# Kernel tuning notes

Measured on AMD Instinct MI355X. Metric: run time of the kernel, lower is better.

The kernel has to match this reference:

```python
import jax, jax.numpy as jnp
import numpy as np
import math

N_HEADS = 16
D_KV = 64
D_MODEL = 1024
NUM_BUCKETS = 32
MAX_DISTANCE = 128


def _relative_position_bucket(rel_pos):
    # encoder (is_decoder=False): bidirectional buckets
    num_buckets = NUM_BUCKETS // 2  # 16
    rel_buckets = (rel_pos > 0).astype(jnp.int32) * num_buckets
    rel_pos = jnp.abs(rel_pos)
    max_exact = num_buckets // 2  # 8
    is_small = rel_pos < max_exact
    rel_pos_large = max_exact + (
        jnp.log(rel_pos.astype(jnp.float32) / max_exact)
        / math.log(MAX_DISTANCE / max_exact)
        * (num_buckets - max_exact)
    ).astype(jnp.int32)
    rel_pos_large = jnp.minimum(rel_pos_large, num_buckets - 1)
    return rel_buckets + jnp.where(is_small, rel_pos, rel_pos_large)


def setup_inputs() -> dict:
    key = jax.random.key(0)
    ks = jax.random.split(key, 6)
    s = 1.0 / math.sqrt(D_MODEL)
    return {
        "hidden_states": jax.random.normal(ks[0], (2, 2048, D_MODEL), jnp.float32),
        "Wq": jax.random.normal(ks[1], (D_MODEL, N_HEADS * D_KV), jnp.float32) * s,
        "Wk": jax.random.normal(ks[2], (D_MODEL, N_HEADS * D_KV), jnp.float32) * s,
        "Wv": jax.random.normal(ks[3], (D_MODEL, N_HEADS * D_KV), jnp.float32) * s,
        "Wo": jax.random.normal(ks[4], (N_HEADS * D_KV, D_MODEL), jnp.float32) * s,
        "rel_bias": jax.random.normal(ks[5], (NUM_BUCKETS, N_HEADS), jnp.float32),
    }


def reference(hidden_states, Wq, Wk, Wv, Wo, rel_bias):
    b, seq, _ = hidden_states.shape
    q = (hidden_states @ Wq).reshape(b, seq, N_HEADS, D_KV)
    k = (hidden_states @ Wk).reshape(b, seq, N_HEADS, D_KV)
    v = (hidden_states @ Wv).reshape(b, seq, N_HEADS, D_KV)

    # relative position bias: [1, n_heads, q_len, k_len]
    ctx = jnp.arange(seq, dtype=jnp.int32)[:, None]
    mem = jnp.arange(seq, dtype=jnp.int32)[None, :]
    buckets = _relative_position_bucket(mem - ctx)  # [q, k]
    pos_bias = rel_bias[buckets]                    # [q, k, h]
    pos_bias = jnp.transpose(pos_bias, (2, 0, 1))[None]  # [1, h, q, k]

    # NOTE: T5-style attention has no 1/sqrt(d) scaling
    attn = jnp.einsum('binc,bjnc->bnij', q, k) + pos_bias
    attn = jax.nn.softmax(attn.astype(jnp.float32), axis=-1).astype(attn.dtype)
    o = jnp.einsum('bnij,bjnc->binc', attn, v).reshape(b, seq, N_HEADS * D_KV)
    return o @ Wo
```

## Files before the change

kernel.cpp:

```cpp
#include <hip/hip_runtime.h>
#include <hip/hip_bf16.h>
#include <math.h>

#define DM   1024
#define HD   1024
#define NH   16
#define DK   64
#define SEQ  2048
#define BATCH 2

typedef __attribute__((ext_vector_type(8))) short bf16x8;
typedef __attribute__((ext_vector_type(4))) float f32x4;

static __device__ __forceinline__ short f2b(float f) {
  union { float f; unsigned u; } v; v.f = f;
  unsigned r = (v.u + 0x7fffu + ((v.u >> 16) & 1u)) >> 16;
  return (short)r;
}

static __device__ __forceinline__ void gload_lds16(const void* g, void* l) {
  __builtin_amdgcn_global_load_lds(
      (const __attribute__((address_space(1))) void*)g,
      (__attribute__((address_space(3))) void*)l, 16, 0, 0);
}


__global__ __launch_bounds__(256) void k_cvt_h(const float* __restrict__ in,
                                               short* __restrict__ out) {
  int i = (blockIdx.x * 256 + threadIdx.x) * 8;
  float4 a = *reinterpret_cast<const float4*>(in + i);
  float4 b = *reinterpret_cast<const float4*>(in + i + 4);
  bf16x8 o;
  o[0] = f2b(a.x); o[1] = f2b(a.y); o[2] = f2b(a.z); o[3] = f2b(a.w);
  o[4] = f2b(b.x); o[5] = f2b(b.y); o[6] = f2b(b.z); o[7] = f2b(b.w);
  *reinterpret_cast<bf16x8*>(out + i) = o;
}

__global__ __launch_bounds__(256) void k_wtrans(const float* __restrict__ Wq,
                                                const float* __restrict__ Wk,
                                                const float* __restrict__ Wv,
                                                const float* __restrict__ Wo,
                                                short* __restrict__ Wts) {
  const float* src = (blockIdx.z == 0) ? Wq : (blockIdx.z == 1) ? Wk
                   : (blockIdx.z == 2) ? Wv : Wo;
  short* dst = Wts + (size_t)blockIdx.z * DM * HD;
  __shared__ float t[32][33];
  int tx = threadIdx.x & 31, ty = threadIdx.x >> 5;
  int k0 = blockIdx.y * 32, n0 = blockIdx.x * 32;
#pragma unroll
  for (int i = 0; i < 4; ++i)
    t[ty + i * 8][tx] = src[(size_t)(k0 + ty + i * 8) * 1024 + n0 + tx];
  __syncthreads();
#pragma unroll
  for (int i = 0; i < 4; ++i)
    dst[(size_t)(n0 + ty + i * 8) * 1024 + k0 + tx] = f2b(t[tx][ty + i * 8]);
}

__global__ __launch_bounds__(256) void k_bias(const float* __restrict__ rel_bias,
                                              float* __restrict__ btab) {
  int idx = blockIdx.x * 256 + threadIdx.x;
  int h = idx >> 12, pos = idx & 4095;
  int delta = pos - 2047;
  int rb = (delta > 0) ? 16 : 0;
  int ar = (delta < 0) ? -delta : delta;
  int bb;
  if (ar < 8) bb = ar;
  else {
    bb = 8 + (int)(logf((float)ar * 0.125f) * (8.0f / 2.7725887222397811f));
    if (bb > 15) bb = 15;
  }
  btab[idx] = rel_bias[(rb + bb) * NH + h];
}

__global__ __launch_bounds__(256) void k_vtrans(const short* __restrict__ Vb,
                                                short* __restrict__ Vt) {
  int bh = blockIdx.y, b = bh >> 4, h = bh & 15;
  int st = blockIdx.x * 64;
  __shared__ short t[64][72];
  int tx = threadIdx.x & 15, ty = threadIdx.x >> 4;
#pragma unroll
  for (int i = 0; i < 4; ++i) {
    int row = ty + i * 16;
    *reinterpret_cast<short4*>(&t[row][tx * 4]) =
        *reinterpret_cast<const short4*>(
            &Vb[(size_t)(b * SEQ + st + row) * HD + h * 64 + tx * 4]);
  }
  __syncthreads();
#pragma unroll
  for (int i = 0; i < 4; ++i) {
    int dk = ty + i * 16;
    short4 v = make_short4(t[tx * 4 + 0][dk], t[tx * 4 + 1][dk],
                           t[tx * 4 + 2][dk], t[tx * 4 + 3][dk]);
    *reinterpret_cast<short4*>(
        &Vt[(size_t)bh * DK * SEQ + (size_t)dk * SEQ + st + tx * 4]) = v;
  }
}

template <int OUTF32>
__global__ __launch_bounds__(256) void k_gemm_bt(const short* __restrict__ A,
                                                 const short* __restrict__ Bt,
                                                 void* __restrict__ Cv,
                                                 size_t btz, size_t cz) {
  __shared__ __align__(16) short As[128 * 32];
  __shared__ __align__(16) short Bs[128 * 32];
  const int tid = threadIdx.x, w = tid >> 6, lane = tid & 63;
  const int wr = w >> 1, wc = w & 1, lg = lane >> 4, l15 = lane & 15;
  const int rowBase = blockIdx.y * 128, colBase = blockIdx.x * 128;
  const short* B = Bt + (size_t)blockIdx.z * btz;

  f32x4 acc[4][4];
#pragma unroll
  for (int m = 0; m < 4; ++m)
#pragma unroll
    for (int n = 0; n < 4; ++n) acc[m][n] = (f32x4){0.f, 0.f, 0.f, 0.f};

  const int c1 = w * 64 + lane, c2 = c1 + 256;
  const short* Ap1 = A + (size_t)(rowBase + (c1 >> 2)) * 1024 + (c1 & 3) * 8;
  const short* Ap2 = A + (size_t)(rowBase + (c2 >> 2)) * 1024 + (c2 & 3) * 8;
  const short* Bp1 = B + (size_t)(colBase + (c1 >> 2)) * 1024 + (c1 & 3) * 8;
  const short* Bp2 = B + (size_t)(colBase + (c2 >> 2)) * 1024 + (c2 & 3) * 8;
  char* AsB = (char*)As;
  char* BsB = (char*)Bs;

  for (int k0 = 0; k0 < 1024; k0 += 32) {
    __syncthreads();
    gload_lds16(Ap1 + k0, AsB + w * 1024);
    gload_lds16(Ap2 + k0, AsB + 4096 + w * 1024);
    gload_lds16(Bp1 + k0, BsB + w * 1024);
    gload_lds16(Bp2 + k0, BsB + 4096 + w * 1024);
    asm volatile("s_waitcnt vmcnt(0)" ::: "memory");
    __syncthreads();
    bf16x8 af[4], bfr[4];
#pragma unroll
    for (int m = 0; m < 4; ++m)
      af[m] = *reinterpret_cast<const bf16x8*>(
          &As[(wr * 64 + m * 16 + l15) * 32 + lg * 8]);
#pragma unroll
    for (int n = 0; n < 4; ++n)
      bfr[n] = *reinterpret_cast<const bf16x8*>(
          &Bs[(wc * 64 + n * 16 + l15) * 32 + lg * 8]);
#pragma unroll
    for (int m = 0; m < 4; ++m)
#pragma unroll
      for (int n = 0; n < 4; ++n)
        acc[m][n] =
            __builtin_amdgcn_mfma_f32_16x16x32_bf16(af[m], bfr[n], acc[m][n], 0, 0, 0);
  }

#pragma unroll
  for (int m = 0; m < 4; ++m)
#pragma unroll
    for (int n = 0; n < 4; ++n) {
      int col = colBase + wc * 64 + n * 16 + l15;
#pragma unroll
      for (int r = 0; r < 4; ++r) {
        int row = rowBase + wr * 64 + m * 16 + lg * 4 + r;
        if (OUTF32)
          ((float*)Cv)[(size_t)row * 1024 + col] = acc[m][n][r];
        else
          ((short*)Cv + (size_t)blockIdx.z * cz)[(size_t)row * 1024 + col] =
              f2b(acc[m][n][r]);
      }
    }
}

static __device__ __forceinline__ void stage_tile(const char* gbase, size_t grs,
                                                  char* lbase, int w, int lane) {
  const int r0 = w * 16 + (lane >> 3);
  const int cb = (lane & 7) * 16;
  const int sw = (r0 & 7) << 4;
  gload_lds16(gbase + (size_t)r0 * grs + (cb ^ sw), lbase + w * 2048);
  gload_lds16(gbase + (size_t)(r0 + 8) * grs + (cb ^ sw), lbase + w * 2048 + 1024);
}

__global__ __launch_bounds__(256, 4) void k_attn(const short* __restrict__ Qb,
                                                 const short* __restrict__ Kb,
                                                 const short* __restrict__ Vt,
                                                 const float* __restrict__ biasTab,
                                                 short* __restrict__ Ob) {
  const int j = blockIdx.x;
  const int orig = (j & 7) * 128 + (j >> 3);
  const int qt = orig & 31, bh = orig >> 5;
  const int b = bh >> 4, h = bh & 15;
  const int w = threadIdx.x >> 6, lane = threadIdx.x & 63;
  const int lg = lane >> 4, l15 = lane & 15;
  const int qbase = qt * 64 + w * 16;

  __shared__ __align__(16) char Ks[2][8192];
  __shared__ __align__(16) char Vs[2][8192];
  __shared__ __align__(16) short Plds[4][1024];
  char* PwB = (char*)(&Plds[w][0]);
  const int swz = (l15 & 7) << 4;

  const short* Qrow = Qb + (size_t)(b * SEQ + qbase + l15) * HD + h * 64 + lg * 8;
  bf16x8 q0 = *reinterpret_cast<const bf16x8*>(Qrow);
  bf16x8 q1 = *reinterpret_cast<const bf16x8*>(Qrow + 32);

  const char* Kg = (const char*)(Kb + (size_t)(b * SEQ) * HD + h * 64);
  const char* Vg = (const char*)(Vt + (size_t)bh * DK * SEQ);
  const float* btab = biasTab + h * 4096 + 2047;
  const float bias_hi = btab[1024];
  const float bias_lo = btab[-1024];

  f32x4 o[4];
#pragma unroll
  for (int c = 0; c < 4; ++c) o[c] = (f32x4){0.f, 0.f, 0.f, 0.f};
  float m_r = -INFINITY, l_r = 0.f;

  const f32x4 z4 = (f32x4){0.f, 0.f, 0.f, 0.f};
  const int rb0 = (l15 * 128 + lg * 16) ^ swz;
  const int rb1 = (l15 * 128 + 64 + lg * 16) ^ swz;

  stage_tile(Kg, 2048, Ks[0], w, lane);
  stage_tile(Vg, 4096, Vs[0], w, lane);
  asm volatile("s_waitcnt vmcnt(0)" ::: "memory");
  __syncthreads();
  int cur = 0;

  for (int kt = 0; kt < 32; ++kt) {
    const int kvb = kt * 64;
    const int dkv = kvb - qbase;
    if (kt < 31) {
      stage_tile(Kg + (size_t)(kvb + 64) * 2048, 2048, Ks[cur ^ 1], w, lane);
      stage_tile(Vg + (size_t)(kvb + 64) * 2, 4096, Vs[cur ^ 1], w, lane);
    }
    const char* KsC = Ks[cur];
    f32x4 s[4];
#pragma unroll
    for (int c = 0; c < 4; ++c) {
      const int krow = c * 16 + l15;
      const int ksw = (krow & 7) << 4;
      const char* kr = KsC + krow * 128;
      bf16x8 kf0 = *reinterpret_cast<const bf16x8*>(kr + ((lg * 16) ^ ksw));
      bf16x8 kf1 = *reinterpret_cast<const bf16x8*>(kr + ((64 + lg * 16) ^ ksw));
      s[c] = __builtin_amdgcn_mfma_f32_16x16x32_bf16(kf0, q0, z4, 0, 0, 0);
      s[c] = __builtin_amdgcn_mfma_f32_16x16x32_bf16(kf1, q1, s[c], 0, 0, 0);
    }
    if (dkv >= 112) {
#pragma unroll
      for (int c = 0; c < 4; ++c)
#pragma unroll
        for (int r = 0; r < 4; ++r) s[c][r] += bias_hi;
    } else if (dkv <= -160) {
#pragma unroll
      for (int c = 0; c < 4; ++c)
#pragma unroll
        for (int r = 0; r < 4; ++r) s[c][r] += bias_lo;
    } else {
#pragma unroll
      for (int c = 0; c < 4; ++c)
#pragma unroll
        for (int r = 0; r < 4; ++r)
          s[c][r] += btab[dkv + c * 16 + lg * 4 + r - l15];
    }
    float mx = s[0][0];
#pragma unroll
    for (int c = 0; c < 4; ++c)
#pragma unroll
      for (int r = 0; r < 4; ++r) mx = fmaxf(mx, s[c][r]);
    mx = fmaxf(mx, __shfl_xor(mx, 16, 64));
    mx = fmaxf(mx, __shfl_xor(mx, 32, 64));
    float mn = fmaxf(m_r, mx);
    float sc = __expf(m_r - mn);
    m_r = mn;
    float rs = 0.f;
#pragma unroll
    for (int c = 0; c < 4; ++c)
#pragma unroll
      for (int r = 0; r < 4; ++r) {
        float p = __expf(s[c][r] - m_r);
        s[c][r] = p;
        rs += p;
      }
    rs += __shfl_xor(rs, 16, 64);
    rs += __shfl_xor(rs, 32, 64);
    l_r = l_r * sc + rs;
#pragma unroll
    for (int c = 0; c < 4; ++c)
#pragma unroll
      for (int r = 0; r < 4; ++r) o[c][r] *= sc;
#pragma unroll
    for (int c = 0; c < 4; ++c) {
      short4 pk;
      pk.x = f2b(s[c][0]); pk.y = f2b(s[c][1]);
      pk.z = f2b(s[c][2]); pk.w = f2b(s[c][3]);
      int byte = (l15 * 128 + c * 32 + lg * 8) ^ swz;
      *reinterpret_cast<short4*>(PwB + byte) = pk;
    }
    const char* VsC = Vs[cur];
    bf16x8 vf0[4], vf1[4];
#pragma unroll
    for (int c = 0; c < 4; ++c) {
      const int vrow = c * 16 + l15;
      const int vsw = (vrow & 7) << 4;
      const char* vr = VsC + vrow * 128;
      vf0[c] = *reinterpret_cast<const bf16x8*>(vr + ((lg * 16) ^ vsw));
      vf1[c] = *reinterpret_cast<const bf16x8*>(vr + ((64 + lg * 16) ^ vsw));
    }
    asm volatile("s_waitcnt lgkmcnt(0)" ::: "memory");
    bf16x8 pb0 = *reinterpret_cast<const bf16x8*>(PwB + rb0);
    bf16x8 pb1 = *reinterpret_cast<const bf16x8*>(PwB + rb1);
#pragma unroll
    for (int c = 0; c < 4; ++c) {
      o[c] = __builtin_amdgcn_mfma_f32_16x16x32_bf16(vf0[c], pb0, o[c], 0, 0, 0);
      o[c] = __builtin_amdgcn_mfma_f32_16x16x32_bf16(vf1[c], pb1, o[c], 0, 0, 0);
    }
    asm volatile("s_waitcnt vmcnt(0)" ::: "memory");
    __syncthreads();
    cur ^= 1;
  }
  float inv = 1.0f / l_r;
  const size_t orow = (size_t)(b * SEQ + qbase + l15) * HD + h * 64;
#pragma unroll
  for (int c = 0; c < 4; ++c) {
    short4 pk;
    pk.x = f2b(o[c][0] * inv); pk.y = f2b(o[c][1] * inv);
    pk.z = f2b(o[c][2] * inv); pk.w = f2b(o[c][3] * inv);
    *reinterpret_cast<short4*>(&Ob[orow + c * 16 + lg * 4]) = pk;
  }
}

extern "C" void kernel_launch(void* const* d_in, const int* in_sizes, int n_in,
                              void* d_out, int out_size, void* d_ws, size_t ws_size,
                              hipStream_t stream) {
  const float* H    = (const float*)d_in[0];
  const float* Wq   = (const float*)d_in[1];
  const float* Wk   = (const float*)d_in[2];
  const float* Wv   = (const float*)d_in[3];
  const float* Wo   = (const float*)d_in[4];
  const float* relb = (const float*)d_in[5];

  char* ws = (char*)d_ws;
  short* Hb   = (short*)(ws);
  short* Wts  = (short*)(ws + ((size_t)8 << 20));
  short* Qb   = (short*)(ws + ((size_t)16 << 20));
  short* Kb   = (short*)(ws + ((size_t)24 << 20));
  short* Vb   = (short*)(ws + ((size_t)32 << 20));
  short* Vt   = (short*)(ws + ((size_t)40 << 20));
  short* Ob   = (short*)(ws + ((size_t)48 << 20));
  float* btab = (float*)(ws + ((size_t)56 << 20));

  k_cvt_h<<<2048, 256, 0, stream>>>(H, Hb);
  k_wtrans<<<dim3(32, 32, 4), 256, 0, stream>>>(Wq, Wk, Wv, Wo, Wts);
  k_bias<<<256, 256, 0, stream>>>(relb, btab);

  k_gemm_bt<0><<<dim3(8, 32, 3), 256, 0, stream>>>(
      Hb, Wts, Qb, (size_t)1024 * 1024, (size_t)4096 * 1024);

  k_vtrans<<<dim3(32, 32), 256, 0, stream>>>(Vb, Vt);
  k_attn<<<1024, 256, 0, stream>>>(Qb, Kb, Vt, btab, Ob);

  k_gemm_bt<1><<<dim3(8, 32, 1), 256, 0, stream>>>(
      Ob, Wts + (size_t)3 * 1024 * 1024, d_out, 0, 0);
}
```

Before: 223.6 us.

## Keep softmax probabilities in registers and use exp2 with lazy rescaling in attention

Folds log2(e) into the Q weight and the bias table so the attention kernel can use exp2 directly. It removes the per-wave LDS round trip for the P matrix by packing probabilities straight into MFMA operands and reading V with a matching permuted layout. It also skips the running-max rescale of the output accumulators unless the new max exceeds the old one by more than a threshold. The LDS footprint and waits shrink, at the cost of more LDS read instructions (short4 loads) for V and a relaxed-max softmax that trusts the threshold to avoid overflow.

```diff
diff --git a/kernel.cpp b/kernel.cpp
--- a/kernel.cpp
+++ b/kernel.cpp
@@ -8,6 +8,8 @@
 #define DK   64
 #define SEQ  2048
 #define BATCH 2
+
+#define LOG2E 1.4426950408889634f
 
 typedef __attribute__((ext_vector_type(8))) short bf16x8;
 typedef __attribute__((ext_vector_type(4))) float f32x4;
@@ -43,6 +45,7 @@
                                                 short* __restrict__ Wts) {
   const float* src = (blockIdx.z == 0) ? Wq : (blockIdx.z == 1) ? Wk
                    : (blockIdx.z == 2) ? Wv : Wo;
+  const float scl = (blockIdx.z == 0) ? LOG2E : 1.0f;
   short* dst = Wts + (size_t)blockIdx.z * DM * HD;
   __shared__ float t[32][33];
   int tx = threadIdx.x & 31, ty = threadIdx.x >> 5;
@@ -53,7 +56,7 @@
   __syncthreads();
 #pragma unroll
   for (int i = 0; i < 4; ++i)
-    dst[(size_t)(n0 + ty + i * 8) * 1024 + k0 + tx] = f2b(t[tx][ty + i * 8]);
+    dst[(size_t)(n0 + ty + i * 8) * 1024 + k0 + tx] = f2b(t[tx][ty + i * 8] * scl);
 }
 
 __global__ __launch_bounds__(256) void k_bias(const float* __restrict__ rel_bias,
@@ -69,7 +72,7 @@
     bb = 8 + (int)(logf((float)ar * 0.125f) * (8.0f / 2.7725887222397811f));
     if (bb > 15) bb = 15;
   }
-  btab[idx] = rel_bias[(rb + bb) * NH + h];
+  btab[idx] = rel_bias[(rb + bb) * NH + h] * LOG2E;
 }
 
 __global__ __launch_bounds__(256) void k_vtrans(const short* __restrict__ Vb,
@@ -188,8 +191,6 @@
 
   __shared__ __align__(16) char Ks[2][8192];
   __shared__ __align__(16) char Vs[2][8192];
-  __shared__ __align__(16) short Plds[4][1024];
-  char* PwB = (char*)(&Plds[w][0]);
   const int swz = (l15 & 7) << 4;
 
   const short* Qrow = Qb + (size_t)(b * SEQ + qbase + l15) * HD + h * 64 + lg * 8;
@@ -208,8 +209,6 @@
   float m_r = -INFINITY, l_r = 0.f;
 
   const f32x4 z4 = (f32x4){0.f, 0.f, 0.f, 0.f};
-  const int rb0 = (l15 * 128 + lg * 16) ^ swz;
-  const int rb1 = (l15 * 128 + 64 + lg * 16) ^ swz;
 
   stage_tile(Kg, 2048, Ks[0], w, lane);
   stage_tile(Vg, 4096, Vs[0], w, lane);
@@ -228,11 +227,9 @@
     f32x4 s[4];
 #pragma unroll
     for (int c = 0; c < 4; ++c) {
-      const int krow = c * 16 + l15;
-      const int ksw = (krow & 7) << 4;
-      const char* kr = KsC + krow * 128;
-      bf16x8 kf0 = *reinterpret_cast<const bf16x8*>(kr + ((lg * 16) ^ ksw));
-      bf16x8 kf1 = *reinterpret_cast<const bf16x8*>(kr + ((64 + lg * 16) ^ ksw));
+      const char* kr = KsC + (c * 16 + l15) * 128;
+      bf16x8 kf0 = *reinterpret_cast<const bf16x8*>(kr + ((lg * 16) ^ swz));
+      bf16x8 kf1 = *reinterpret_cast<const bf16x8*>(kr + ((64 + lg * 16) ^ swz));
       s[c] = __builtin_amdgcn_mfma_f32_16x16x32_bf16(kf0, q0, z4, 0, 0, 0);
       s[c] = __builtin_amdgcn_mfma_f32_16x16x32_bf16(kf1, q1, s[c], 0, 0, 0);
     }
@@ -253,57 +250,58 @@
         for (int r = 0; r < 4; ++r)
           s[c][r] += btab[dkv + c * 16 + lg * 4 + r - l15];
     }
-    float mx = s[0][0];
-#pragma unroll
-    for (int c = 0; c < 4; ++c)
-#pragma unroll
-      for (int r = 0; r < 4; ++r) mx = fmaxf(mx, s[c][r]);
+    float t0 = fmaxf(fmaxf(s[0][0], s[0][1]), fmaxf(s[0][2], s[0][3]));
+    float t1 = fmaxf(fmaxf(s[1][0], s[1][1]), fmaxf(s[1][2], s[1][3]));
+    float t2 = fmaxf(fmaxf(s[2][0], s[2][1]), fmaxf(s[2][2], s[2][3]));
+    float t3 = fmaxf(fmaxf(s[3][0], s[3][1]), fmaxf(s[3][2], s[3][3]));
+    float mx = fmaxf(fmaxf(t0, t1), fmaxf(t2, t3));
     mx = fmaxf(mx, __shfl_xor(mx, 16, 64));
     mx = fmaxf(mx, __shfl_xor(mx, 32, 64));
-    float mn = fmaxf(m_r, mx);
-    float sc = __expf(m_r - mn);
-    m_r = mn;
-    float rs = 0.f;
+    if (!__all(mx <= m_r + 8.0f)) {
+      float mn = fmaxf(m_r, mx);
+      float sc = __builtin_exp2f(m_r - mn);
+      m_r = mn;
+      l_r *= sc;
+#pragma unroll
+      for (int c = 0; c < 4; ++c)
+#pragma unroll
+        for (int r = 0; r < 4; ++r) o[c][r] *= sc;
+    }
 #pragma unroll
     for (int c = 0; c < 4; ++c)
 #pragma unroll
-      for (int r = 0; r < 4; ++r) {
-        float p = __expf(s[c][r] - m_r);
-        s[c][r] = p;
-        rs += p;
-      }
+      for (int r = 0; r < 4; ++r) s[c][r] = __builtin_exp2f(s[c][r] - m_r);
+    float r0 = (s[0][0] + s[0][1]) + (s[0][2] + s[0][3]);
+    float r1 = (s[1][0] + s[1][1]) + (s[1][2] + s[1][3]);
+    float r2 = (s[2][0] + s[2][1]) + (s[2][2] + s[2][3]);
+    float r3 = (s[3][0] + s[3][1]) + (s[3][2] + s[3][3]);
+    float rs = (r0 + r1) + (r2 + r3);
     rs += __shfl_xor(rs, 16, 64);
     rs += __shfl_xor(rs, 32, 64);
-    l_r = l_r * sc + rs;
-#pragma unroll
-    for (int c = 0; c < 4; ++c)
-#pragma unroll
-      for (int r = 0; r < 4; ++r) o[c][r] *= sc;
-#pragma unroll
-    for (int c = 0; c < 4; ++c) {
-      short4 pk;
-      pk.x = f2b(s[c][0]); pk.y = f2b(s[c][1]);
-      pk.z = f2b(s[c][2]); pk.w = f2b(s[c][3]);
-      int byte = (l15 * 128 + c * 32 + lg * 8) ^ swz;
-      *reinterpret_cast<short4*>(PwB + byte) = pk;
+    l_r += rs;
+    bf16x8 pb0, pb1;
+#pragma unroll
+    for (int r = 0; r < 4; ++r) {
+      pb0[r]     = f2b(s[0][r]);
+      pb0[4 + r] = f2b(s[1][r]);
+      pb1[r]     = f2b(s[2][r]);
+      pb1[4 + r] = f2b(s[3][r]);
     }
     const char* VsC = Vs[cur];
-    bf16x8 vf0[4], vf1[4];
-#pragma unroll
-    for (int c = 0; c < 4; ++c) {
-      const int vrow = c * 16 + l15;
-      const int vsw = (vrow & 7) << 4;
-      const char* vr = VsC + vrow * 128;
-      vf0[c] = *reinterpret_cast<const bf16x8*>(vr + ((lg * 16) ^ vsw));
-      vf1[c] = *reinterpret_cast<const bf16x8*>(vr + ((64 + lg * 16) ^ vsw));
-    }
-    asm volatile("s_waitcnt lgkmcnt(0)" ::: "memory");
-    bf16x8 pb0 = *reinterpret_cast<const bf16x8*>(PwB + rb0);
-    bf16x8 pb1 = *reinterpret_cast<const bf16x8*>(PwB + rb1);
-#pragma unroll
-    for (int c = 0; c < 4; ++c) {
-      o[c] = __builtin_amdgcn_mfma_f32_16x16x32_bf16(vf0[c], pb0, o[c], 0, 0, 0);
-      o[c] = __builtin_amdgcn_mfma_f32_16x16x32_bf16(vf1[c], pb1, o[c], 0, 0, 0);
+#pragma unroll
+    for (int d = 0; d < 4; ++d) {
+      const char* vr = VsC + (d * 16 + l15) * 128;
+      short4 a0 = *reinterpret_cast<const short4*>(vr + ((lg * 8) ^ swz));
+      short4 a1 = *reinterpret_cast<const short4*>(vr + ((32 + lg * 8) ^ swz));
+      short4 b0 = *reinterpret_cast<const short4*>(vr + ((64 + lg * 8) ^ swz));
+      short4 b1 = *reinterpret_cast<const short4*>(vr + ((96 + lg * 8) ^ swz));
+      bf16x8 v0, v1;
+      v0[0] = a0.x; v0[1] = a0.y; v0[2] = a0.z; v0[3] = a0.w;
+      v0[4] = a1.x; v0[5] = a1.y; v0[6] = a1.z; v0[7] = a1.w;
+      v1[0] = b0.x; v1[1] = b0.y; v1[2] = b0.z; v1[3] = b0.w;
+      v1[4] = b1.x; v1[5] = b1.y; v1[6] = b1.z; v1[7] = b1.w;
+      o[d] = __builtin_amdgcn_mfma_f32_16x16x32_bf16(v0, pb0, o[d], 0, 0, 0);
+      o[d] = __builtin_amdgcn_mfma_f32_16x16x32_bf16(v1, pb1, o[d], 0, 0, 0);
     }
     asm volatile("s_waitcnt vmcnt(0)" ::: "memory");
     __syncthreads();
@@ -312,11 +310,11 @@
   float inv = 1.0f / l_r;
   const size_t orow = (size_t)(b * SEQ + qbase + l15) * HD + h * 64;
 #pragma unroll
-  for (int c = 0; c < 4; ++c) {
+  for (int d = 0; d < 4; ++d) {
     short4 pk;
-    pk.x = f2b(o[c][0] * inv); pk.y = f2b(o[c][1] * inv);
-    pk.z = f2b(o[c][2] * inv); pk.w = f2b(o[c][3] * inv);
-    *reinterpret_cast<short4*>(&Ob[orow + c * 16 + lg * 4]) = pk;
+    pk.x = f2b(o[d][0] * inv); pk.y = f2b(o[d][1] * inv);
+    pk.z = f2b(o[d][2] * inv); pk.w = f2b(o[d][3] * inv);
+    *reinterpret_cast<short4*>(&Ob[orow + d * 16 + lg * 4]) = pk;
   }
 }
 
```

Result: slower. 240.0 us (+7.3%).
